# Kernel tuning notes

Hardware: AMD Instinct MI355X
Metric: run time of the kernel (lower is better)

Reference implementation:

```python
import jax, jax.numpy as jnp
import numpy as np

B, D, O = 8192, 64, 256

def setup_inputs() -> dict:
    key = jax.random.key(0)
    k1, k2, k3 = jax.random.split(key, 3)
    x = jax.random.normal(k1, (B, D), dtype=jnp.float32)
    centers = jax.random.uniform(k2, (O, 1, D), dtype=jnp.float32)  # RandomUniform(0,1)
    # Original uses Constant(10.0) which saturates exp(-quad) to 0; use small random
    # betas so the quadratic form is in a numerically meaningful range.
    betas = jax.random.normal(k3, (O, D, D), dtype=jnp.float32) * 0.05
    return {"x": x, "centers": centers, "betas": betas}

def reference(x, centers, betas):
    # precision[o] = betas[o] @ betas[o]^T   -> [O, D, D]
    precision = jnp.einsum('ode,ofe->odf', betas, betas)
    # diff[o,b,:] = centers[o] - x[b]        -> [O, B, D]
    diff = centers - x[None, :, :]
    # quad[o,b] = diff[o,b]^T P[o] diff[o,b] -> [O, B]
    quad = jnp.einsum('obd,odf,obf->ob', diff, precision, diff)
    return jnp.exp(-quad).T  # [B, O]
```

## Files before the change

### kernel.cpp

```cpp
#include <hip/hip_runtime.h>
#include <hip/hip_bf16.h>

typedef __bf16 bf16x8 __attribute__((ext_vector_type(8)));
typedef float  f32x4  __attribute__((ext_vector_type(4)));
typedef float  f32x16 __attribute__((ext_vector_type(16)));

constexpr int Bn = 8192, Dn = 64, On = 256;

#define GLD16(g, l) __builtin_amdgcn_global_load_lds( \
    (const __attribute__((address_space(1))) void*)(g), \
    (__attribute__((address_space(3))) void*)(l), 16, 0, 0)
#define GLD4(g, l) __builtin_amdgcn_global_load_lds( \
    (const __attribute__((address_space(1))) void*)(g), \
    (__attribute__((address_space(3))) void*)(l), 4, 0, 0)

__global__ void k_prep(const float* __restrict__ betas, const float* __restrict__ centers,
                       __bf16* __restrict__ bTsw, float* __restrict__ ncpk) {
    __shared__ float s[64 * 65];
    const int o = blockIdx.x, tid = threadIdx.x;
    const float* bo = betas + (size_t)o * 4096;
    for (int j = tid; j < 1024; j += 256) {
        int d = j >> 4, e4 = (j & 15) * 4;
        float4 v = ((const float4*)bo)[j];
        s[d * 65 + e4 + 0] = v.x; s[d * 65 + e4 + 1] = v.y;
        s[d * 65 + e4 + 2] = v.z; s[d * 65 + e4 + 3] = v.w;
    }
    __syncthreads();
    for (int j = tid; j < 4096; j += 256) {
        int e = j >> 6, dpos = j & 63;
        int slot = dpos >> 3, jj = dpos & 7;
        int d = ((slot ^ (e & 7)) << 3) + jj;
        bTsw[(size_t)o * 4096 + j] = (__bf16)s[d * 65 + e];
    }
    if (tid < 64) {
        int et = tid >> 5, rem = tid & 31, l5 = rem >> 4, reg = rem & 15;
        int row = et * 32 + l5 * 4 + (reg & 3) + ((reg >> 2) << 3);
        float acc = 0.f;
        for (int d = 0; d < 64; ++d) acc += s[d * 65 + row] * centers[o * 64 + d];
        ncpk[o * 64 + tid] = -acc;
    }
}

__global__ void __launch_bounds__(256)
__attribute__((amdgpu_waves_per_eu(2, 2)))
k_main(const float* __restrict__ x, const __bf16* __restrict__ bTsw,
       const float* __restrict__ ncpk, float* __restrict__ out) {
    __shared__ __align__(16) __bf16 sX[128 * 64];
    __shared__ __align__(16) __bf16 sA[4][64 * 64];
    __shared__ __align__(16) float  sCp[4][64];

    const int tid = threadIdx.x, wq = tid >> 6, lane = tid & 63;
    const int l31 = lane & 31, l5 = lane >> 5;
    const int bbase = blockIdx.x * 128;
    const int o0 = blockIdx.y * 32 + wq * 8;

#pragma unroll
    for (int i = 0; i < 4; ++i) {
        int id = i * 256 + tid, rb = id >> 3, c = id & 7;
        const float* xp = x + (size_t)(bbase + rb) * 64 + c * 8;
        float4 v0 = *(const float4*)xp, v1 = *(const float4*)(xp + 4);
        bf16x8 f;
        f[0] = (__bf16)v0.x; f[1] = (__bf16)v0.y; f[2] = (__bf16)v0.z; f[3] = (__bf16)v0.w;
        f[4] = (__bf16)v1.x; f[5] = (__bf16)v1.y; f[6] = (__bf16)v1.z; f[7] = (__bf16)v1.w;
        *(bf16x8*)(sX + rb * 64 + ((c ^ (rb & 7)) << 3)) = f;
    }
    __syncthreads();

    bf16x8 xf[4][4];
#pragma unroll
    for (int bt = 0; bt < 4; ++bt)
#pragma unroll
        for (int k = 0; k < 4; ++k) {
            int row = bt * 32 + l31, c = k * 2 + l5;
            xf[bt][k] = *(const bf16x8*)(sX + row * 64 + ((c ^ (row & 7)) << 3));
        }

    __bf16* myA  = &sA[wq][0];
    float*  myCp = &sCp[wq][0];

    for (int oi = 0; oi < 8; ++oi) {
        const int o = o0 + oi;
        const __bf16* gA = bTsw + (size_t)o * 4096 + lane * 8;
#pragma unroll
        for (int cll = 0; cll < 8; ++cll)
            GLD16(gA + cll * 512, myA + cll * 512);
        GLD4(ncpk + o * 64 + lane, myCp);
        __builtin_amdgcn_sched_barrier(0);
        __builtin_amdgcn_s_waitcnt(0x0f70);
        __builtin_amdgcn_sched_barrier(0);

        f32x4 qv[4] = {{0.f,0.f,0.f,0.f},{0.f,0.f,0.f,0.f},{0.f,0.f,0.f,0.f},{0.f,0.f,0.f,0.f}};
#pragma unroll
        for (int et = 0; et < 2; ++et) {
            f32x16 cpv;
#pragma unroll
            for (int r4 = 0; r4 < 4; ++r4)
                ((f32x4*)&cpv)[r4] = *(const f32x4*)(myCp + et * 32 + l5 * 16 + r4 * 4);
            bf16x8 af[4];
#pragma unroll
            for (int k = 0; k < 4; ++k) {
                int row = et * 32 + l31, c = k * 2 + l5;
                af[k] = *(const bf16x8*)(myA + row * 64 + ((c ^ (row & 7)) << 3));
            }
#pragma unroll
            for (int bt = 0; bt < 4; ++bt) {
                f32x16 acc = __builtin_amdgcn_mfma_f32_32x32x16_bf16(af[0], xf[bt][0], cpv, 0, 0, 0);
                acc = __builtin_amdgcn_mfma_f32_32x32x16_bf16(af[1], xf[bt][1], acc, 0, 0, 0);
                acc = __builtin_amdgcn_mfma_f32_32x32x16_bf16(af[2], xf[bt][2], acc, 0, 0, 0);
                acc = __builtin_amdgcn_mfma_f32_32x32x16_bf16(af[3], xf[bt][3], acc, 0, 0, 0);
#pragma unroll
                for (int j = 0; j < 16; ++j)
                    qv[bt][j & 3] = fmaf(acc[j], acc[j], qv[bt][j & 3]);
            }
        }
        float q[4];
#pragma unroll
        for (int bt = 0; bt < 4; ++bt) {
            float qs = (qv[bt][0] + qv[bt][1]) + (qv[bt][2] + qv[bt][3]);
            qs += __shfl_xor(qs, 32, 64);
            q[bt] = qs;
        }
        float qA = l5 ? q[2] : q[0], qB = l5 ? q[3] : q[1];
        int bA = bbase + l5 * 64 + l31;
        out[(size_t)bA * 256 + o]        = __expf(-qA);
        out[(size_t)(bA + 32) * 256 + o] = __expf(-qB);
        __builtin_amdgcn_sched_barrier(0);
    }
}

extern "C" void kernel_launch(void* const* d_in, const int* in_sizes, int n_in,
                              void* d_out, int out_size, void* d_ws, size_t ws_size,
                              hipStream_t stream) {
    const float* x       = (const float*)d_in[0];
    const float* centers = (const float*)d_in[1];
    const float* betas   = (const float*)d_in[2];
    float* out = (float*)d_out;

    char* ws = (char*)d_ws;
    __bf16* bTsw = (__bf16*)ws;
    float*  ncpk = (float*)(ws + 2 * (1 << 20));

    k_prep<<<dim3(On),           dim3(256), 0, stream>>>(betas, centers, bTsw, ncpk);
    k_main<<<dim3(Bn / 128, On / 32), dim3(256), 0, stream>>>(x, bTsw, ncpk, out);
}
```

Before: 88.19 us.

## Load A fragments directly to registers with double-buffered prefetch and vectorized stores

The prep kernel now writes betas in MFMA fragment order so each lane loads its A operands straight from global memory into registers. The LDS staging and per-iteration waitcnt stall are gone. The next o's fragments are prefetched into a second register set while the current one computes. All ncpk values are loaded once up front, and outputs are gathered into float4 vectors for wider stores. This raises register pressure under the 2-waves-per-EU bound and relies on the compiler to keep the prefetch overlapped.

```diff
diff --git a/kernel.cpp b/kernel.cpp
--- a/kernel.cpp
+++ b/kernel.cpp
@@ -10,12 +10,9 @@
 #define GLD16(g, l) __builtin_amdgcn_global_load_lds( \
     (const __attribute__((address_space(1))) void*)(g), \
     (__attribute__((address_space(3))) void*)(l), 16, 0, 0)
-#define GLD4(g, l) __builtin_amdgcn_global_load_lds( \
-    (const __attribute__((address_space(1))) void*)(g), \
-    (__attribute__((address_space(3))) void*)(l), 4, 0, 0)
 
 __global__ void k_prep(const float* __restrict__ betas, const float* __restrict__ centers,
-                       __bf16* __restrict__ bTsw, float* __restrict__ ncpk) {
+                       __bf16* __restrict__ bTf, float* __restrict__ ncpk) {
     __shared__ float s[64 * 65];
     const int o = blockIdx.x, tid = threadIdx.x;
     const float* bo = betas + (size_t)o * 4096;
@@ -27,10 +24,10 @@
     }
     __syncthreads();
     for (int j = tid; j < 4096; j += 256) {
-        int e = j >> 6, dpos = j & 63;
-        int slot = dpos >> 3, jj = dpos & 7;
-        int d = ((slot ^ (e & 7)) << 3) + jj;
-        bTsw[(size_t)o * 4096 + j] = (__bf16)s[d * 65 + e];
+        int f = j >> 9, l = (j >> 3) & 63, jj = j & 7;
+        int e = ((f >> 2) << 5) + (l & 31);
+        int d = (((f & 3) << 1) + (l >> 5)) * 8 + jj;
+        bTf[(size_t)o * 4096 + j] = (__bf16)s[d * 65 + e];
     }
     if (tid < 64) {
         int et = tid >> 5, rem = tid & 31, l5 = rem >> 4, reg = rem & 15;
@@ -41,18 +38,65 @@
     }
 }
 
+template <int OI>
+__device__ __forceinline__ void ldA(const __bf16* __restrict__ gA, bf16x8 (&af)[8]) {
+#pragma unroll
+    for (int f = 0; f < 8; ++f)
+        af[f] = *(const bf16x8*)(gA + OI * 4096 + f * 512);
+}
+
+template <int OI>
+__device__ __forceinline__ void step(const float* __restrict__ cpw, const bf16x8 (&af)[8],
+                                     const bf16x8 (&xf)[4][4], int l5,
+                                     f32x4 (&eA)[2], f32x4 (&eB)[2]) {
+    f32x4 qv[4] = {{0.f,0.f,0.f,0.f},{0.f,0.f,0.f,0.f},{0.f,0.f,0.f,0.f},{0.f,0.f,0.f,0.f}};
+#pragma unroll
+    for (int et = 0; et < 2; ++et) {
+        f32x16 cpv;
+#pragma unroll
+        for (int r4 = 0; r4 < 4; ++r4)
+            ((f32x4*)&cpv)[r4] = *(const f32x4*)(cpw + OI * 64 + et * 32 + l5 * 16 + r4 * 4);
+#pragma unroll
+        for (int bt = 0; bt < 4; ++bt) {
+            f32x16 acc = __builtin_amdgcn_mfma_f32_32x32x16_bf16(af[et*4+0], xf[bt][0], cpv, 0, 0, 0);
+            acc = __builtin_amdgcn_mfma_f32_32x32x16_bf16(af[et*4+1], xf[bt][1], acc, 0, 0, 0);
+            acc = __builtin_amdgcn_mfma_f32_32x32x16_bf16(af[et*4+2], xf[bt][2], acc, 0, 0, 0);
+            acc = __builtin_amdgcn_mfma_f32_32x32x16_bf16(af[et*4+3], xf[bt][3], acc, 0, 0, 0);
+#pragma unroll
+            for (int j = 0; j < 16; ++j)
+                qv[bt][j & 3] = fmaf(acc[j], acc[j], qv[bt][j & 3]);
+        }
+    }
+    float q[4];
+#pragma unroll
+    for (int bt = 0; bt < 4; ++bt) {
+        float qs = (qv[bt][0] + qv[bt][1]) + (qv[bt][2] + qv[bt][3]);
+        qs += __shfl_xor(qs, 32, 64);
+        q[bt] = qs;
+    }
+    float qA = l5 ? q[2] : q[0], qB = l5 ? q[3] : q[1];
+    eA[OI >> 2][OI & 3] = __expf(-qA);
+    eB[OI >> 2][OI & 3] = __expf(-qB);
+}
+
 __global__ void __launch_bounds__(256)
 __attribute__((amdgpu_waves_per_eu(2, 2)))
-k_main(const float* __restrict__ x, const __bf16* __restrict__ bTsw,
+k_main(const float* __restrict__ x, const __bf16* __restrict__ bTf,
        const float* __restrict__ ncpk, float* __restrict__ out) {
     __shared__ __align__(16) __bf16 sX[128 * 64];
-    __shared__ __align__(16) __bf16 sA[4][64 * 64];
-    __shared__ __align__(16) float  sCp[4][64];
+    __shared__ __align__(16) float  sCp[4][512];
 
     const int tid = threadIdx.x, wq = tid >> 6, lane = tid & 63;
     const int l31 = lane & 31, l5 = lane >> 5;
     const int bbase = blockIdx.x * 128;
     const int o0 = blockIdx.y * 32 + wq * 8;
+
+    GLD16(ncpk + o0 * 64 + lane * 4, &sCp[wq][0]);
+    GLD16(ncpk + o0 * 64 + 256 + lane * 4, &sCp[wq][256]);
+
+    const __bf16* gA = bTf + (size_t)o0 * 4096 + (size_t)lane * 8;
+    bf16x8 a0[8], a1[8];
+    ldA<0>(gA, a0);
 
 #pragma unroll
     for (int i = 0; i < 4; ++i) {
@@ -75,57 +119,31 @@
             xf[bt][k] = *(const bf16x8*)(sX + row * 64 + ((c ^ (row & 7)) << 3));
         }
 
-    __bf16* myA  = &sA[wq][0];
-    float*  myCp = &sCp[wq][0];
+    const float* cpw = &sCp[wq][0];
+    f32x4 eA[2], eB[2];
 
-    for (int oi = 0; oi < 8; ++oi) {
-        const int o = o0 + oi;
-        const __bf16* gA = bTsw + (size_t)o * 4096 + lane * 8;
-#pragma unroll
-        for (int cll = 0; cll < 8; ++cll)
-            GLD16(gA + cll * 512, myA + cll * 512);
-        GLD4(ncpk + o * 64 + lane, myCp);
-        __builtin_amdgcn_sched_barrier(0);
-        __builtin_amdgcn_s_waitcnt(0x0f70);
-        __builtin_amdgcn_sched_barrier(0);
+    ldA<1>(gA, a1); step<0>(cpw, a0, xf, l5, eA, eB);
+    __builtin_amdgcn_sched_barrier(0);
+    ldA<2>(gA, a0); step<1>(cpw, a1, xf, l5, eA, eB);
+    __builtin_amdgcn_sched_barrier(0);
+    ldA<3>(gA, a1); step<2>(cpw, a0, xf, l5, eA, eB);
+    __builtin_amdgcn_sched_barrier(0);
+    ldA<4>(gA, a0); step<3>(cpw, a1, xf, l5, eA, eB);
+    __builtin_amdgcn_sched_barrier(0);
+    ldA<5>(gA, a1); step<4>(cpw, a0, xf, l5, eA, eB);
+    __builtin_amdgcn_sched_barrier(0);
+    ldA<6>(gA, a0); step<5>(cpw, a1, xf, l5, eA, eB);
+    __builtin_amdgcn_sched_barrier(0);
+    ldA<7>(gA, a1); step<6>(cpw, a0, xf, l5, eA, eB);
+    __builtin_amdgcn_sched_barrier(0);
+    step<7>(cpw, a1, xf, l5, eA, eB);
 
-        f32x4 qv[4] = {{0.f,0.f,0.f,0.f},{0.f,0.f,0.f,0.f},{0.f,0.f,0.f,0.f},{0.f,0.f,0.f,0.f}};
-#pragma unroll
-        for (int et = 0; et < 2; ++et) {
-            f32x16 cpv;
-#pragma unroll
-            for (int r4 = 0; r4 < 4; ++r4)
-                ((f32x4*)&cpv)[r4] = *(const f32x4*)(myCp + et * 32 + l5 * 16 + r4 * 4);
-            bf16x8 af[4];
-#pragma unroll
-            for (int k = 0; k < 4; ++k) {
-                int row = et * 32 + l31, c = k * 2 + l5;
-                af[k] = *(const bf16x8*)(myA + row * 64 + ((c ^ (row & 7)) << 3));
-            }
-#pragma unroll
-            for (int bt = 0; bt < 4; ++bt) {
-                f32x16 acc = __builtin_amdgcn_mfma_f32_32x32x16_bf16(af[0], xf[bt][0], cpv, 0, 0, 0);
-                acc = __builtin_amdgcn_mfma_f32_32x32x16_bf16(af[1], xf[bt][1], acc, 0, 0, 0);
-                acc = __builtin_amdgcn_mfma_f32_32x32x16_bf16(af[2], xf[bt][2], acc, 0, 0, 0);
-                acc = __builtin_amdgcn_mfma_f32_32x32x16_bf16(af[3], xf[bt][3], acc, 0, 0, 0);
-#pragma unroll
-                for (int j = 0; j < 16; ++j)
-                    qv[bt][j & 3] = fmaf(acc[j], acc[j], qv[bt][j & 3]);
-            }
-        }
-        float q[4];
-#pragma unroll
-        for (int bt = 0; bt < 4; ++bt) {
-            float qs = (qv[bt][0] + qv[bt][1]) + (qv[bt][2] + qv[bt][3]);
-            qs += __shfl_xor(qs, 32, 64);
-            q[bt] = qs;
-        }
-        float qA = l5 ? q[2] : q[0], qB = l5 ? q[3] : q[1];
-        int bA = bbase + l5 * 64 + l31;
-        out[(size_t)bA * 256 + o]        = __expf(-qA);
-        out[(size_t)(bA + 32) * 256 + o] = __expf(-qB);
-        __builtin_amdgcn_sched_barrier(0);
-    }
+    const int bA = bbase + l5 * 64 + l31;
+    float* op = out + (size_t)bA * 256 + o0;
+    *(f32x4*)(op)                = eA[0];
+    *(f32x4*)(op + 4)            = eA[1];
+    *(f32x4*)(op + 32 * 256)     = eB[0];
+    *(f32x4*)(op + 32 * 256 + 4) = eB[1];
 }
 
 extern "C" void kernel_launch(void* const* d_in, const int* in_sizes, int n_in,
@@ -137,9 +155,9 @@
     float* out = (float*)d_out;
 
     char* ws = (char*)d_ws;
-    __bf16* bTsw = (__bf16*)ws;
+    __bf16* bTf  = (__bf16*)ws;
     float*  ncpk = (float*)(ws + 2 * (1 << 20));
 
-    k_prep<<<dim3(On),           dim3(256), 0, stream>>>(betas, centers, bTsw, ncpk);
-    k_main<<<dim3(Bn / 128, On / 32), dim3(256), 0, stream>>>(x, bTsw, ncpk, out);
+    k_prep<<<dim3(On),                dim3(256), 0, stream>>>(betas, centers, bTf, ncpk);
+    k_main<<<dim3(Bn / 128, On / 32), dim3(256), 0, stream>>>(x, bTf, ncpk, out);
 }
```

After: 84.20 us. -4.5%, faster.

## Restructure main kernel: shared double-buffered betas across waves, vectorized output stores

Applied to the files above, without the earlier changes.

The main kernel now has each block cover 8 outputs instead of 32. The four waves split the 128 batch rows and share one double-buffered LDS copy of each output's transformed beta, prefetching the next output while computing the current one. Betas are stored in an MFMA-fragment-ready layout so LDS reads are linear. Results are collected in registers and written as one float4 per lane instead of scattered scalar stores. The prep kernel vectorizes its writes and splits the center projection across all threads. In exchange, the grid is four times larger, x is reloaded and converted four times as often, and a block-wide barrier is added per output.

```diff
diff --git a/kernel.cpp b/kernel.cpp
--- a/kernel.cpp
+++ b/kernel.cpp
@@ -10,13 +10,11 @@
 #define GLD16(g, l) __builtin_amdgcn_global_load_lds( \
     (const __attribute__((address_space(1))) void*)(g), \
     (__attribute__((address_space(3))) void*)(l), 16, 0, 0)
-#define GLD4(g, l) __builtin_amdgcn_global_load_lds( \
-    (const __attribute__((address_space(1))) void*)(g), \
-    (__attribute__((address_space(3))) void*)(l), 4, 0, 0)
 
 __global__ void k_prep(const float* __restrict__ betas, const float* __restrict__ centers,
-                       __bf16* __restrict__ bTsw, float* __restrict__ ncpk) {
+                       __bf16* __restrict__ bTf, float* __restrict__ ncpk) {
     __shared__ float s[64 * 65];
+    __shared__ float red[256];
     const int o = blockIdx.x, tid = threadIdx.x;
     const float* bo = betas + (size_t)o * 4096;
     for (int j = tid; j < 1024; j += 256) {
@@ -26,33 +24,48 @@
         s[d * 65 + e4 + 2] = v.z; s[d * 65 + e4 + 3] = v.w;
     }
     __syncthreads();
-    for (int j = tid; j < 4096; j += 256) {
-        int e = j >> 6, dpos = j & 63;
-        int slot = dpos >> 3, jj = dpos & 7;
-        int d = ((slot ^ (e & 7)) << 3) + jj;
-        bTsw[(size_t)o * 4096 + j] = (__bf16)s[d * 65 + e];
+    for (int ch = tid; ch < 512; ch += 256) {
+        int f = ch >> 6, l = ch & 63;
+        int e  = ((f >> 2) << 5) + (l & 31);
+        int db = (((f & 3) << 1) + (l >> 5)) * 8;
+        bf16x8 v;
+#pragma unroll
+        for (int jj = 0; jj < 8; ++jj) v[jj] = (__bf16)s[(db + jj) * 65 + e];
+        *(bf16x8*)(bTf + (size_t)o * 4096 + ch * 8) = v;
     }
-    if (tid < 64) {
-        int et = tid >> 5, rem = tid & 31, l5 = rem >> 4, reg = rem & 15;
-        int row = et * 32 + l5 * 4 + (reg & 3) + ((reg >> 2) << 3);
+    {
+        int t = tid & 63, part = tid >> 6;
+        int et = t >> 5, rem = t & 31, l5r = rem >> 4, reg = rem & 15;
+        int row = et * 32 + l5r * 4 + (reg & 3) + ((reg >> 2) << 3);
         float acc = 0.f;
-        for (int d = 0; d < 64; ++d) acc += s[d * 65 + row] * centers[o * 64 + d];
-        ncpk[o * 64 + tid] = -acc;
+#pragma unroll
+        for (int d = part * 16; d < part * 16 + 16; ++d)
+            acc += s[d * 65 + row] * centers[o * 64 + d];
+        red[part * 64 + t] = acc;
     }
+    __syncthreads();
+    if (tid < 64)
+        ncpk[o * 64 + tid] = -(red[tid] + red[64 + tid] + red[128 + tid] + red[192 + tid]);
 }
 
-__global__ void __launch_bounds__(256)
-__attribute__((amdgpu_waves_per_eu(2, 2)))
-k_main(const float* __restrict__ x, const __bf16* __restrict__ bTsw,
+__global__ void __launch_bounds__(256, 4)
+k_main(const float* __restrict__ x, const __bf16* __restrict__ bTf,
        const float* __restrict__ ncpk, float* __restrict__ out) {
     __shared__ __align__(16) __bf16 sX[128 * 64];
-    __shared__ __align__(16) __bf16 sA[4][64 * 64];
-    __shared__ __align__(16) float  sCp[4][64];
+    __shared__ __align__(16) __bf16 sA[2][4096];
+    __shared__ __align__(16) float  sCp[512];
 
     const int tid = threadIdx.x, wq = tid >> 6, lane = tid & 63;
     const int l31 = lane & 31, l5 = lane >> 5;
     const int bbase = blockIdx.x * 128;
-    const int o0 = blockIdx.y * 32 + wq * 8;
+    const int o0 = blockIdx.y * 8;
+
+    const __bf16* gA = bTf + (size_t)o0 * 4096;
+    const int sl = wq * 1024;
+
+    GLD16(gA + sl + lane * 8,       &sA[0][sl]);
+    GLD16(gA + sl + 512 + lane * 8, &sA[0][sl + 512]);
+    if (wq < 2) GLD16(ncpk + o0 * 64 + wq * 256 + lane * 4, sCp + wq * 256);
 
 #pragma unroll
     for (int i = 0; i < 4; ++i) {
@@ -66,66 +79,52 @@
     }
     __syncthreads();
 
-    bf16x8 xf[4][4];
+    bf16x8 xf[4];
 #pragma unroll
-    for (int bt = 0; bt < 4; ++bt)
+    for (int k = 0; k < 4; ++k) {
+        int row = wq * 32 + l31, c = k * 2 + l5;
+        xf[k] = *(const bf16x8*)(sX + row * 64 + ((c ^ (row & 7)) << 3));
+    }
+
+    f32x4 e0 = {0.f, 0.f, 0.f, 0.f}, e1 = {0.f, 0.f, 0.f, 0.f};
 #pragma unroll
-        for (int k = 0; k < 4; ++k) {
-            int row = bt * 32 + l31, c = k * 2 + l5;
-            xf[bt][k] = *(const bf16x8*)(sX + row * 64 + ((c ^ (row & 7)) << 3));
+    for (int oi = 0; oi < 8; ++oi) {
+        const __bf16* cb = &sA[oi & 1][0];
+        if (oi < 7) {
+            __bf16* nb = &sA[(oi + 1) & 1][0];
+            GLD16(gA + (oi + 1) * 4096 + sl + lane * 8,       nb + sl);
+            GLD16(gA + (oi + 1) * 4096 + sl + 512 + lane * 8, nb + sl + 512);
+            __builtin_amdgcn_sched_barrier(0);
         }
-
-    __bf16* myA  = &sA[wq][0];
-    float*  myCp = &sCp[wq][0];
-
-    for (int oi = 0; oi < 8; ++oi) {
-        const int o = o0 + oi;
-        const __bf16* gA = bTsw + (size_t)o * 4096 + lane * 8;
-#pragma unroll
-        for (int cll = 0; cll < 8; ++cll)
-            GLD16(gA + cll * 512, myA + cll * 512);
-        GLD4(ncpk + o * 64 + lane, myCp);
-        __builtin_amdgcn_sched_barrier(0);
-        __builtin_amdgcn_s_waitcnt(0x0f70);
-        __builtin_amdgcn_sched_barrier(0);
-
-        f32x4 qv[4] = {{0.f,0.f,0.f,0.f},{0.f,0.f,0.f,0.f},{0.f,0.f,0.f,0.f},{0.f,0.f,0.f,0.f}};
+        f32x4 qv = {0.f, 0.f, 0.f, 0.f};
 #pragma unroll
         for (int et = 0; et < 2; ++et) {
             f32x16 cpv;
 #pragma unroll
             for (int r4 = 0; r4 < 4; ++r4)
-                ((f32x4*)&cpv)[r4] = *(const f32x4*)(myCp + et * 32 + l5 * 16 + r4 * 4);
+                ((f32x4*)&cpv)[r4] = *(const f32x4*)(sCp + oi * 64 + et * 32 + l5 * 16 + r4 * 4);
             bf16x8 af[4];
 #pragma unroll
-            for (int k = 0; k < 4; ++k) {
-                int row = et * 32 + l31, c = k * 2 + l5;
-                af[k] = *(const bf16x8*)(myA + row * 64 + ((c ^ (row & 7)) << 3));
-            }
+            for (int k = 0; k < 4; ++k)
+                af[k] = *(const bf16x8*)(cb + (et * 4 + k) * 512 + lane * 8);
+            f32x16 acc = __builtin_amdgcn_mfma_f32_32x32x16_bf16(af[0], xf[0], cpv, 0, 0, 0);
+            acc = __builtin_amdgcn_mfma_f32_32x32x16_bf16(af[1], xf[1], acc, 0, 0, 0);
+            acc = __builtin_amdgcn_mfma_f32_32x32x16_bf16(af[2], xf[2], acc, 0, 0, 0);
+            acc = __builtin_amdgcn_mfma_f32_32x32x16_bf16(af[3], xf[3], acc, 0, 0, 0);
 #pragma unroll
-            for (int bt = 0; bt < 4; ++bt) {
-                f32x16 acc = __builtin_amdgcn_mfma_f32_32x32x16_bf16(af[0], xf[bt][0], cpv, 0, 0, 0);
-                acc = __builtin_amdgcn_mfma_f32_32x32x16_bf16(af[1], xf[bt][1], acc, 0, 0, 0);
-                acc = __builtin_amdgcn_mfma_f32_32x32x16_bf16(af[2], xf[bt][2], acc, 0, 0, 0);
-                acc = __builtin_amdgcn_mfma_f32_32x32x16_bf16(af[3], xf[bt][3], acc, 0, 0, 0);
-#pragma unroll
-                for (int j = 0; j < 16; ++j)
-                    qv[bt][j & 3] = fmaf(acc[j], acc[j], qv[bt][j & 3]);
-            }
+            for (int j = 0; j < 16; ++j)
+                qv[j & 3] = fmaf(acc[j], acc[j], qv[j & 3]);
         }
-        float q[4];
-#pragma unroll
-        for (int bt = 0; bt < 4; ++bt) {
-            float qs = (qv[bt][0] + qv[bt][1]) + (qv[bt][2] + qv[bt][3]);
-            qs += __shfl_xor(qs, 32, 64);
-            q[bt] = qs;
-        }
-        float qA = l5 ? q[2] : q[0], qB = l5 ? q[3] : q[1];
-        int bA = bbase + l5 * 64 + l31;
-        out[(size_t)bA * 256 + o]        = __expf(-qA);
-        out[(size_t)(bA + 32) * 256 + o] = __expf(-qB);
-        __builtin_amdgcn_sched_barrier(0);
+        float qs = (qv[0] + qv[1]) + (qv[2] + qv[3]);
+        qs += __shfl_xor(qs, 32, 64);
+        float ev = __expf(-qs);
+        if (oi < 4) e0[oi] = ev; else e1[oi - 4] = ev;
+        if (oi < 7) __syncthreads();
     }
+
+    const int b = bbase + wq * 32 + l31;
+    float* op = out + (size_t)b * 256 + o0 + l5 * 4;
+    *(f32x4*)op = l5 ? e1 : e0;
 }
 
 extern "C" void kernel_launch(void* const* d_in, const int* in_sizes, int n_in,
@@ -137,9 +136,9 @@
     float* out = (float*)d_out;
 
     char* ws = (char*)d_ws;
-    __bf16* bTsw = (__bf16*)ws;
+    __bf16* bTf  = (__bf16*)ws;
     float*  ncpk = (float*)(ws + 2 * (1 << 20));
 
-    k_prep<<<dim3(On),           dim3(256), 0, stream>>>(betas, centers, bTsw, ncpk);
-    k_main<<<dim3(Bn / 128, On / 32), dim3(256), 0, stream>>>(x, bTsw, ncpk, out);
+    k_prep<<<dim3(On),               dim3(256), 0, stream>>>(betas, centers, bTf, ncpk);
+    k_main<<<dim3(Bn / 128, On / 8), dim3(256), 0, stream>>>(x, bTf, ncpk, out);
 }
```

Measured after the change: 85.84 us. 2.7% less time.
